# Optimization experiments

Hardware: AMD Instinct MI355X
Metric: run time of the kernel (lower is better)

Reference implementation:

```python
import jax, jax.numpy as jnp
import numpy as np

B, N, M = 4, 2048, 2048
DIM = 1024
HEADS = 16
DIM_HEAD = 64
INNER = HEADS * DIM_HEAD
SCALE = 8.0


def layer_norm(x, g, eps=1e-5):
    mean = jnp.mean(x, axis=-1, keepdims=True)
    var = jnp.mean((x - mean) ** 2, axis=-1, keepdims=True)
    return (x - mean) * jax.lax.rsqrt(var + eps) * g


def l2norm(t, eps=1e-12):
    n = jnp.maximum(jnp.linalg.norm(t, axis=-1, keepdims=True), eps)
    return t / n


def setup_inputs() -> dict:
    key = jax.random.key(0)
    ks = jax.random.split(key, 8)
    x = jax.random.normal(ks[0], (B, N, DIM), dtype=jnp.float32)
    context = jax.random.normal(ks[1], (B, M, DIM), dtype=jnp.float32)
    # parameters
    g_norm = jnp.ones((DIM,), dtype=jnp.float32)
    null_kv = jax.random.normal(ks[2], (2, DIM_HEAD), dtype=jnp.float32)
    Wq = jax.random.normal(ks[3], (DIM, INNER), dtype=jnp.float32) / np.sqrt(DIM)
    Wkv = jax.random.normal(ks[4], (DIM, 2 * INNER), dtype=jnp.float32) / np.sqrt(DIM)
    q_scale = jnp.ones((DIM_HEAD,), dtype=jnp.float32)
    k_scale = jnp.ones((DIM_HEAD,), dtype=jnp.float32)
    Wout = jax.random.normal(ks[5], (INNER, DIM), dtype=jnp.float32) / np.sqrt(INNER)
    g_out = jnp.ones((DIM,), dtype=jnp.float32)
    return {"x": x, "context": context, "g_norm": g_norm, "null_kv": null_kv,
            "Wq": Wq, "Wkv": Wkv, "q_scale": q_scale, "k_scale": k_scale,
            "Wout": Wout, "g_out": g_out}


def reference(x, context, g_norm, null_kv, Wq, Wkv, q_scale, k_scale, Wout, g_out):
    b = x.shape[0]
    xn = layer_norm(x, g_norm)            # [b, n, dim]
    ctx = context                          # norm_context=False -> Identity
    q = xn @ Wq                            # [b, n, inner]
    kv = ctx @ Wkv                         # [b, m, 2*inner]
    k, v = jnp.split(kv, 2, axis=-1)
    split_heads = lambda t: t.reshape(b, t.shape[1], HEADS, DIM_HEAD).transpose(0, 2, 1, 3)
    q, k, v = map(split_heads, (q, k, v))  # [b, h, n|m, d]
    # null kv token prepended along the key/value sequence dim
    nk = jnp.broadcast_to(null_kv[0], (b, HEADS, 1, DIM_HEAD))
    nv = jnp.broadcast_to(null_kv[1], (b, HEADS, 1, DIM_HEAD))
    k = jnp.concatenate([nk, k], axis=2)   # [b, h, m+1, d]
    v = jnp.concatenate([nv, v], axis=2)
    # QK-norm with learned per-dim scales
    q = l2norm(q) * q_scale
    k = l2norm(k) * k_scale
    sim = jnp.einsum('bhid,bhjd->bhij', q, k) * SCALE
    attn = jax.nn.softmax(sim.astype(jnp.float32), axis=-1).astype(sim.dtype)
    out = jnp.einsum('bhij,bhjd->bhid', attn, v)
    out = out.transpose(0, 2, 1, 3).reshape(b, -1, INNER)  # [b, n, inner]
    out = out @ Wout
    return layer_norm(out, g_out)
```

## Files before the change

### kernel.cpp

```cpp
#include <hip/hip_runtime.h>

#define BATCH 4
#define NSEQ 2048
#define MSEQ 2048
#define DIM 1024
#define HEADS 16
#define DHEAD 64
#define INNER 1024
#define KVLEN 2049
#define KVPAD 2176

typedef unsigned short u16;
typedef unsigned int u32;
typedef __bf16 bf16x8 __attribute__((ext_vector_type(8)));
typedef float f32x4 __attribute__((ext_vector_type(4)));

__device__ inline u16 f2bf(float f) {
  u32 u = __builtin_bit_cast(u32, f);
  u = (u + 0x7fffu + ((u >> 16) & 1u)) >> 16;
  return (u16)u;
}
__device__ inline float bf2f(u16 x) {
  return __builtin_bit_cast(float, (u32)x << 16);
}
__device__ inline u32 pk_bf16(float lo, float hi) {
  u32 r;
  asm("v_cvt_pk_bf16_f32 %0, %1, %2" : "=v"(r) : "v"(lo), "v"(hi));
  return r;
}

__device__ __forceinline__ void gld_lds16(const void* g, void* l) {
  __builtin_amdgcn_global_load_lds(
      (const __attribute__((address_space(1))) void*)g,
      (__attribute__((address_space(3))) void*)l, 16, 0, 0);
}

template <bool OUT_BF16>
__global__ __launch_bounds__(256) void ln_kernel(const float* __restrict__ x,
                                                 const float* __restrict__ g,
                                                 void* __restrict__ out) {
  const int row = blockIdx.x;
  const int t = threadIdx.x;
  const float4 v = ((const float4*)(x + (size_t)row * 1024))[t];
  float sum = v.x + v.y + v.z + v.w;
  float sq = v.x * v.x + v.y * v.y + v.z * v.z + v.w * v.w;
  for (int m = 1; m < 64; m <<= 1) {
    sum += __shfl_xor(sum, m, 64);
    sq += __shfl_xor(sq, m, 64);
  }
  __shared__ float red[8];
  const int w = t >> 6, l = t & 63;
  if (l == 0) { red[w] = sum; red[4 + w] = sq; }
  __syncthreads();
  sum = red[0] + red[1] + red[2] + red[3];
  sq = red[4] + red[5] + red[6] + red[7];
  const float mean = sum * (1.0f / 1024.0f);
  const float var = sq * (1.0f / 1024.0f) - mean * mean;
  const float rstd = rsqrtf(var + 1e-5f);
  const float4 gv = ((const float4*)g)[t];
  float o0 = (v.x - mean) * rstd * gv.x;
  float o1 = (v.y - mean) * rstd * gv.y;
  float o2 = (v.z - mean) * rstd * gv.z;
  float o3 = (v.w - mean) * rstd * gv.w;
  if (OUT_BF16) {
    ushort4 ov;
    ov.x = f2bf(o0); ov.y = f2bf(o1); ov.z = f2bf(o2); ov.w = f2bf(o3);
    ((ushort4*)((u16*)out + (size_t)row * 1024))[t] = ov;
  } else {
    float4 ov;
    ov.x = o0; ov.y = o1; ov.z = o2; ov.w = o3;
    ((float4*)((float*)out + (size_t)row * 1024))[t] = ov;
  }
}

__global__ __launch_bounds__(256) void cast_bf16(const float* __restrict__ in,
                                                 u16* __restrict__ out, int n4) {
  int i = blockIdx.x * 256 + threadIdx.x;
  if (i < n4) {
    float4 v = ((const float4*)in)[i];
    ushort4 o;
    o.x = f2bf(v.x); o.y = f2bf(v.y); o.z = f2bf(v.z); o.w = f2bf(v.w);
    ((ushort4*)out)[i] = o;
  }
}

__global__ __launch_bounds__(256) void transpose_cast(const float* __restrict__ W,
                                                      u16* __restrict__ WT, int K, int N) {
  __shared__ float tile[32][33];
  const int tx = threadIdx.x & 31, ty = threadIdx.x >> 5;
  const int k0 = blockIdx.y * 32, n0 = blockIdx.x * 32;
  for (int r = ty; r < 32; r += 8) tile[r][tx] = W[(size_t)(k0 + r) * N + n0 + tx];
  __syncthreads();
  for (int r = ty; r < 32; r += 8) WT[(size_t)(n0 + r) * K + k0 + tx] = f2bf(tile[tx][r]);
}

template <int MODE>
__global__ __launch_bounds__(256) void gemm_bt(const u16* __restrict__ A,
                                               const u16* __restrict__ Bt,
                                               void* __restrict__ Cv,
                                               int M, int N, int K,
                                               const float* __restrict__ scale,
                                               u16* __restrict__ aux) {
  __shared__ __align__(16) u16 As[128 * 32];
  __shared__ __align__(16) u16 Bs[128 * 32];
  const int t = threadIdx.x;
  const int w = t >> 6, l = t & 63, l15 = l & 15, lq = l >> 4;
  const int m0 = blockIdx.y * 128, n0 = blockIdx.x * 128;
  const int wm = (w >> 1) * 64, wn = (w & 1) * 64;
  const int lr = l >> 2;
  const int lo = (l & 3) * 8;
  f32x4 acc[4][4] = {};
  for (int k0 = 0; k0 < K; k0 += 32) {
#pragma unroll
    for (int it = 0; it < 2; it++) {
      const int row = (w * 2 + it) * 16 + lr;
      gld_lds16(&A[(size_t)(m0 + row) * K + k0 + lo], &As[row * 32 + lo]);
      gld_lds16(&Bt[(size_t)(n0 + row) * K + k0 + lo], &Bs[row * 32 + lo]);
    }
    __syncthreads();
    bf16x8 af[4], bfr[4];
#pragma unroll
    for (int i = 0; i < 4; i++) af[i] = *(bf16x8*)&As[(wm + i * 16 + l15) * 32 + lq * 8];
#pragma unroll
    for (int j = 0; j < 4; j++) bfr[j] = *(bf16x8*)&Bs[(wn + j * 16 + l15) * 32 + lq * 8];
#pragma unroll
    for (int i = 0; i < 4; i++)
#pragma unroll
      for (int j = 0; j < 4; j++)
        acc[i][j] = __builtin_amdgcn_mfma_f32_16x16x32_bf16(af[i], bfr[j], acc[i][j], 0, 0, 0);
    __syncthreads();
  }

  if (MODE <= 1) {
#pragma unroll
    for (int i = 0; i < 4; i++)
#pragma unroll
      for (int j = 0; j < 4; j++)
#pragma unroll
        for (int r = 0; r < 4; r++) {
          const size_t off =
              (size_t)(m0 + wm + i * 16 + lq * 4 + r) * N + n0 + wn + j * 16 + l15;
          if (MODE == 1) ((u16*)Cv)[off] = f2bf(acc[i][j][r]);
          else ((float*)Cv)[off] = acc[i][j][r];
        }
    return;
  }

  const int head = (n0 + wn) >> 6;
  if (MODE == 3 && head >= 16) {
#pragma unroll
    for (int i = 0; i < 4; i++)
#pragma unroll
      for (int j = 0; j < 4; j++)
#pragma unroll
        for (int r = 0; r < 4; r++) {
          const int row = m0 + wm + i * 16 + lq * 4 + r;
          aux[(size_t)row * 1024 + (head - 16) * 64 + j * 16 + l15] = f2bf(acc[i][j][r]);
        }
    return;
  }
  float sc[4];
#pragma unroll
  for (int j = 0; j < 4; j++) sc[j] = scale[j * 16 + l15];
  const float mul = (MODE == 2) ? 8.0f : 1.0f;
  u16* outp = (u16*)Cv;
#pragma unroll
  for (int i = 0; i < 4; i++)
#pragma unroll
    for (int r = 0; r < 4; r++) {
      float ss = 0.f;
#pragma unroll
      for (int j = 0; j < 4; j++) ss = fmaf(acc[i][j][r], acc[i][j][r], ss);
#pragma unroll
      for (int m = 1; m < 16; m <<= 1) ss += __shfl_xor(ss, m, 64);
      const float inv = mul / fmaxf(sqrtf(ss), 1e-12f);
      const int row = m0 + wm + i * 16 + lq * 4 + r;
      const int b = row >> 11, n = row & 2047;
      const size_t base = (MODE == 2)
          ? (((size_t)b * 16 + head) * 2048 + n) * 64
          : (((size_t)b * 16 + head) * (size_t)KVPAD + n + 1) * 64;
#pragma unroll
      for (int j = 0; j < 4; j++)
        outp[base + j * 16 + l15] = f2bf(acc[i][j][r] * inv * sc[j]);
    }
}

__global__ __launch_bounds__(256) void v_post(const u16* __restrict__ vg,
                                              u16* __restrict__ vt) {
  __shared__ u16 tile[64][68];
  const int bh = blockIdx.y, mt = blockIdx.x;
  const int tx = threadIdx.x & 63, ty = threadIdx.x >> 6;
  const int b = bh >> 4, h = bh & 15;
  const int m0 = mt * 64;
  for (int r = ty; r < 64; r += 4)
    tile[tx][r] = vg[(size_t)(b * 2048 + m0 + r) * 1024 + h * 64 + tx];
  __syncthreads();
  const int abs_ = 1 + m0 + tx;
  const int slot = (abs_ & ~127) | ((abs_ & 15) << 3) | ((abs_ >> 4) & 7);
  for (int d = ty; d < 64; d += 4)
    vt[((size_t)bh * 64 + d) * KVPAD + slot] = tile[d][tx];
}

__global__ __launch_bounds__(256) void null_tail(const float* __restrict__ null_kv,
                                                 const float* __restrict__ k_scale,
                                                 u16* __restrict__ kn, u16* __restrict__ vt) {
  const int bh = blockIdx.x, t = threadIdx.x;
  const int d = t & 63, seg = t >> 6;
  if (seg == 0) {
    float nk = null_kv[d];
    float nv = null_kv[64 + d];
    float ss = nk * nk;
    for (int m = 1; m < 64; m <<= 1) ss += __shfl_xor(ss, m, 64);
    float inv = 1.0f / fmaxf(sqrtf(ss), 1e-12f);
    kn[((size_t)bh * KVPAD) * 64 + d] = f2bf(nk * inv * k_scale[d]);
    vt[((size_t)bh * 64 + d) * KVPAD] = f2bf(nv);
  }
  for (int m = KVLEN + seg; m < KVPAD; m += 4) kn[((size_t)bh * KVPAD + m) * 64 + d] = 0;
  u16* vrow = vt + ((size_t)bh * 64 + d) * KVPAD;
  for (int m = KVLEN + seg; m < KVPAD; m += 4) vrow[m] = 0;
}

__global__ __launch_bounds__(256, 4) void attn_kernel(const u16* __restrict__ qn,
                                                      const u16* __restrict__ kn,
                                                      const u16* __restrict__ vt,
                                                      u16* __restrict__ aout) {
  __shared__ __align__(16) u16 Ks[128 * 64];
  __shared__ __align__(16) u16 Vs[64 * 128];
  const int qt = blockIdx.x, bh = blockIdx.y;
  const int b = bh >> 4, h = bh & 15;
  const int t = threadIdx.x, w = t >> 6, l = t & 63, l15 = l & 15, lq = l >> 4;

  bf16x8 aqf[2];
  {
    const u16* qrow = qn + ((size_t)bh * 2048 + qt * 64 + w * 16 + l15) * 64 + lq * 8;
    aqf[0] = *(const bf16x8*)(qrow);
    aqf[1] = *(const bf16x8*)(qrow + 32);
  }

  int so[4];
#pragma unroll
  for (int ks = 0; ks < 4; ks++) so[ks] = ((ks * 4 + lq) ^ (l15 & 7)) * 8;

  const u16* kn_b = kn + (size_t)bh * KVPAD * 64;
  const u16* vt_b = vt + (size_t)bh * 64 * KVPAD;
  const u16* ksrc[4];
  const u16* vsrc[4];
#pragma unroll
  for (int i = 0; i < 4; i++) {
    const int rk = (w * 4 + i) * 8 + (l >> 3);
    const int sk = (l & 7) ^ ((l >> 3) & 7);
    ksrc[i] = kn_b + rk * 64 + sk * 8;
    const int rd = (w * 4 + i) * 4 + (l >> 4);
    const int sv = (l & 15) ^ (rd & 7);
    vsrc[i] = vt_b + (size_t)rd * KVPAD + sv * 8;
  }
  u16* kdst = &Ks[w * 2048 + l * 8];
  u16* vdst = &Vs[w * 2048 + l * 8];

  f32x4 O[4] = {};
  float lsum[4] = {0.f, 0.f, 0.f, 0.f};
  const float LOG2E = 1.44269504f;
  const float MBIAS = -8.0f * 1.44269504f;

  for (int kt = 0; kt < 17; kt++) {
#pragma unroll
    for (int i = 0; i < 4; i++) {
      gld_lds16(ksrc[i] + kt * 8192, kdst + i * 512);
      gld_lds16(vsrc[i] + kt * 128, vdst + i * 512);
    }
    __syncthreads();

    f32x4 S[8] = {};
    __builtin_amdgcn_s_setprio(1);
#pragma unroll
    for (int ks = 0; ks < 2; ks++)
#pragma unroll
      for (int j = 0; j < 8; j++) {
        bf16x8 bk = *(bf16x8*)&Ks[(j * 16 + l15) * 64 + so[ks]];
        S[j] = __builtin_amdgcn_mfma_f32_16x16x32_bf16(aqf[ks], bk, S[j], 0, 0, 0);
      }
    __builtin_amdgcn_s_setprio(0);
    __syncthreads();

    const bool last = (kt == 16);
#pragma unroll
    for (int r = 0; r < 4; r++) {
      float pe[8];
#pragma unroll
      for (int j = 0; j < 8; j++) {
        float p = __builtin_amdgcn_exp2f(fmaf(S[j][r], LOG2E, MBIAS));
        if (last && ((j << 4) | l15) != 0) p = 0.f;
        lsum[r] += p;
        pe[j] = p;
      }
      uint4 pw;
      pw.x = pk_bf16(pe[0], pe[1]);
      pw.y = pk_bf16(pe[2], pe[3]);
      pw.z = pk_bf16(pe[4], pe[5]);
      pw.w = pk_bf16(pe[6], pe[7]);
      const int prow = w * 16 + lq * 4 + r;
      *(uint4*)&Ks[prow * 128 + ((l15 ^ (prow & 7)) * 8)] = pw;
    }

    __builtin_amdgcn_s_setprio(1);
#pragma unroll
    for (int ks = 0; ks < 4; ks++) {
      bf16x8 ap = *(bf16x8*)&Ks[(w * 16 + l15) * 128 + so[ks]];
#pragma unroll
      for (int nt = 0; nt < 4; nt++) {
        bf16x8 bv = *(bf16x8*)&Vs[(nt * 16 + l15) * 128 + so[ks]];
        O[nt] = __builtin_amdgcn_mfma_f32_16x16x32_bf16(ap, bv, O[nt], 0, 0, 0);
      }
    }
    __builtin_amdgcn_s_setprio(0);
    __syncthreads();
  }

#pragma unroll
  for (int r = 0; r < 4; r++)
#pragma unroll
    for (int m = 1; m < 16; m <<= 1) lsum[r] += __shfl_xor(lsum[r], m, 64);
#pragma unroll
  for (int nt = 0; nt < 4; nt++)
#pragma unroll
    for (int r = 0; r < 4; r++) {
      int row = qt * 64 + w * 16 + lq * 4 + r;
      int col = h * 64 + nt * 16 + l15;
      float val = O[nt][r] / lsum[r];
      aout[((size_t)b * 2048 + row) * 1024 + col] = f2bf(val);
    }
}

extern "C" void kernel_launch(void* const* d_in, const int* in_sizes, int n_in,
                              void* d_out, int out_size, void* d_ws, size_t ws_size,
                              hipStream_t stream) {
  const float* x = (const float*)d_in[0];
  const float* context = (const float*)d_in[1];
  const float* g_norm = (const float*)d_in[2];
  const float* null_kv = (const float*)d_in[3];
  const float* Wq = (const float*)d_in[4];
  const float* Wkv = (const float*)d_in[5];
  const float* q_scale = (const float*)d_in[6];
  const float* k_scale = (const float*)d_in[7];
  const float* Wout = (const float*)d_in[8];
  const float* g_out = (const float*)d_in[9];
  float* out = (float*)d_out;

  char* ws = (char*)d_ws;
  u16* xn = (u16*)(ws);
  u16* ctxb = (u16*)(ws + 16777216);
  u16* wqT = (u16*)(ws + 33554432);
  u16* wkvT = (u16*)(ws + 35651584);
  u16* woutT = (u16*)(ws + 39845888);
  u16* qnb = (u16*)(ws + 41943040);
  u16* knb = (u16*)(ws + 58720256);
  u16* vtb = (u16*)(ws + 76546048);
  u16* vg = (u16*)(ws + 94371840);
  float* outg = (float*)(ws + 111149056);
  u16* attn_out = vg;

  ln_kernel<true><<<8192, 256, 0, stream>>>(x, g_norm, xn);
  cast_bf16<<<8192, 256, 0, stream>>>(context, ctxb, 2097152);
  transpose_cast<<<dim3(32, 32), 256, 0, stream>>>(Wq, wqT, 1024, 1024);
  transpose_cast<<<dim3(64, 32), 256, 0, stream>>>(Wkv, wkvT, 1024, 2048);
  transpose_cast<<<dim3(32, 32), 256, 0, stream>>>(Wout, woutT, 1024, 1024);
  gemm_bt<2><<<dim3(8, 64), 256, 0, stream>>>(xn, wqT, qnb, 8192, 1024, 1024, q_scale, nullptr);
  gemm_bt<3><<<dim3(16, 64), 256, 0, stream>>>(ctxb, wkvT, knb, 8192, 2048, 1024, k_scale, vg);
  v_post<<<dim3(32, 64), 256, 0, stream>>>(vg, vtb);
  null_tail<<<64, 256, 0, stream>>>(null_kv, k_scale, knb, vtb);
  attn_kernel<<<dim3(32, 64), 256, 0, stream>>>(qnb, knb, vtb, attn_out);
  gemm_bt<0><<<dim3(8, 64), 256, 0, stream>>>(attn_out, woutT, outg, 8192, 1024, 1024, nullptr, nullptr);
  ln_kernel<false><<<8192, 256, 0, stream>>>(outg, g_out, out);
}
```

Before: 420.4 us.

## Compute transposed QK^T so probabilities stay in registers for the PV MFMA

The score MFMA now uses K as the A operand and Q as the B operand, so each lane holds a column of S^T, which matches the A-operand layout the P·V MFMA needs. Probabilities are packed into bf16 registers directly instead of going through LDS, which removes one LDS store, one LDS load and a barrier per tile. The V transpose permutation in v_post changes to match the new key ordering, and the row sums are reduced with a different shuffle pattern. The risk is that the new key permutation and mask indexing must line up exactly with the MFMA output layout.

```diff
diff --git a/kernel.cpp b/kernel.cpp
--- a/kernel.cpp
+++ b/kernel.cpp
@@ -196,7 +196,8 @@
     tile[tx][r] = vg[(size_t)(b * 2048 + m0 + r) * 1024 + h * 64 + tx];
   __syncthreads();
   const int abs_ = 1 + m0 + tx;
-  const int slot = (abs_ & ~127) | ((abs_ & 15) << 3) | ((abs_ >> 4) & 7);
+  const int a = abs_ & 127;
+  const int slot = (abs_ & ~127) | (a & 0x63) | ((a & 0x10) >> 2) | ((a & 0x0C) << 1);
   for (int d = ty; d < 64; d += 4)
     vt[((size_t)bh * 64 + d) * KVPAD + slot] = tile[d][tx];
 }
@@ -258,7 +259,7 @@
   u16* vdst = &Vs[w * 2048 + l * 8];
 
   f32x4 O[4] = {};
-  float lsum[4] = {0.f, 0.f, 0.f, 0.f};
+  float lsum = 0.f;
   const float LOG2E = 1.44269504f;
   const float MBIAS = -8.0f * 1.44269504f;
 
@@ -270,63 +271,64 @@
     }
     __syncthreads();
 
-    f32x4 S[8] = {};
+    f32x4 St[8] = {};
     __builtin_amdgcn_s_setprio(1);
 #pragma unroll
     for (int ks = 0; ks < 2; ks++)
 #pragma unroll
       for (int j = 0; j < 8; j++) {
-        bf16x8 bk = *(bf16x8*)&Ks[(j * 16 + l15) * 64 + so[ks]];
-        S[j] = __builtin_amdgcn_mfma_f32_16x16x32_bf16(aqf[ks], bk, S[j], 0, 0, 0);
+        bf16x8 ak = *(bf16x8*)&Ks[(j * 16 + l15) * 64 + so[ks]];
+        St[j] = __builtin_amdgcn_mfma_f32_16x16x32_bf16(ak, aqf[ks], St[j], 0, 0, 0);
+      }
+    __builtin_amdgcn_s_setprio(0);
+
+    const bool last = (kt == 16);
+    float p[8][4];
+#pragma unroll
+    for (int j = 0; j < 8; j++)
+#pragma unroll
+      for (int r = 0; r < 4; r++) {
+        float pv = __builtin_amdgcn_exp2f(fmaf(St[j][r], LOG2E, MBIAS));
+        if (last && ((j << 4) + (lq << 2) + r) != 0) pv = 0.f;
+        lsum += pv;
+        p[j][r] = pv;
+      }
+    bf16x8 pa[4];
+#pragma unroll
+    for (int m = 0; m < 4; m++) {
+      uint4 pw;
+      pw.x = pk_bf16(p[2 * m][0], p[2 * m][1]);
+      pw.y = pk_bf16(p[2 * m][2], p[2 * m][3]);
+      pw.z = pk_bf16(p[2 * m + 1][0], p[2 * m + 1][1]);
+      pw.w = pk_bf16(p[2 * m + 1][2], p[2 * m + 1][3]);
+      pa[m] = __builtin_bit_cast(bf16x8, pw);
+    }
+
+    __builtin_amdgcn_s_setprio(1);
+#pragma unroll
+    for (int m = 0; m < 4; m++)
+#pragma unroll
+      for (int nt = 0; nt < 4; nt++) {
+        bf16x8 bv = *(bf16x8*)&Vs[(nt * 16 + l15) * 128 + so[m]];
+        O[nt] = __builtin_amdgcn_mfma_f32_16x16x32_bf16(pa[m], bv, O[nt], 0, 0, 0);
       }
     __builtin_amdgcn_s_setprio(0);
     __syncthreads();
-
-    const bool last = (kt == 16);
-#pragma unroll
-    for (int r = 0; r < 4; r++) {
-      float pe[8];
-#pragma unroll
-      for (int j = 0; j < 8; j++) {
-        float p = __builtin_amdgcn_exp2f(fmaf(S[j][r], LOG2E, MBIAS));
-        if (last && ((j << 4) | l15) != 0) p = 0.f;
-        lsum[r] += p;
-        pe[j] = p;
-      }
-      uint4 pw;
-      pw.x = pk_bf16(pe[0], pe[1]);
-      pw.y = pk_bf16(pe[2], pe[3]);
-      pw.z = pk_bf16(pe[4], pe[5]);
-      pw.w = pk_bf16(pe[6], pe[7]);
-      const int prow = w * 16 + lq * 4 + r;
-      *(uint4*)&Ks[prow * 128 + ((l15 ^ (prow & 7)) * 8)] = pw;
-    }
-
-    __builtin_amdgcn_s_setprio(1);
-#pragma unroll
-    for (int ks = 0; ks < 4; ks++) {
-      bf16x8 ap = *(bf16x8*)&Ks[(w * 16 + l15) * 128 + so[ks]];
-#pragma unroll
-      for (int nt = 0; nt < 4; nt++) {
-        bf16x8 bv = *(bf16x8*)&Vs[(nt * 16 + l15) * 128 + so[ks]];
-        O[nt] = __builtin_amdgcn_mfma_f32_16x16x32_bf16(ap, bv, O[nt], 0, 0, 0);
-      }
-    }
-    __builtin_amdgcn_s_setprio(0);
-    __syncthreads();
-  }
-
-#pragma unroll
-  for (int r = 0; r < 4; r++)
-#pragma unroll
-    for (int m = 1; m < 16; m <<= 1) lsum[r] += __shfl_xor(lsum[r], m, 64);
+  }
+
+  lsum += __shfl_xor(lsum, 16, 64);
+  lsum += __shfl_xor(lsum, 32, 64);
+  float ls[4];
+#pragma unroll
+  for (int r = 0; r < 4; r++) ls[r] = __shfl(lsum, lq * 4 + r, 64);
+
 #pragma unroll
   for (int nt = 0; nt < 4; nt++)
 #pragma unroll
     for (int r = 0; r < 4; r++) {
       int row = qt * 64 + w * 16 + lq * 4 + r;
       int col = h * 64 + nt * 16 + l15;
-      float val = O[nt][r] / lsum[r];
+      float val = O[nt][r] / ls[r];
       aout[((size_t)b * 2048 + row) * 1024 + col] = f2bf(val);
     }
 }
```

Result: faster. 405.4 us (-3.6%).
